# Kernel tuning notes

Hardware: AMD Instinct MI355X
Metric: run time of the kernel (lower is better)

## Reference

```python
import jax, jax.numpy as jnp
import numpy as np

N, D, M, E, K = 16384, 512, 1024, 8, 2
LOSS_COEF = 0.01
EPS = 1e-10


def setup_inputs() -> dict:
    key = jax.random.key(0)
    ks = jax.random.split(key, 6)
    x = jax.random.normal(ks[0], (N, D), dtype=jnp.float32)
    # gate weight (torch init is zeros; use small random so routing is non-degenerate)
    w_gate = 0.02 * jax.random.normal(ks[1], (D, E), dtype=jnp.float32)
    # stacked expert FFN params: Linear(D->M), GELU, Linear(M->D)
    W1 = jax.random.normal(ks[2], (E, D, M), dtype=jnp.float32) / np.sqrt(D)
    b1 = jnp.zeros((E, M), dtype=jnp.float32)
    W2 = jax.random.normal(ks[3], (E, M, D), dtype=jnp.float32) / np.sqrt(M)
    b2 = jnp.zeros((E, D), dtype=jnp.float32)
    return {"x": x, "w_gate": w_gate, "W1": W1, "b1": b1, "W2": W2, "b2": b2}


def _cv_squared(v):
    # torch .var() is unbiased (ddof=1)
    v = v.astype(jnp.float32)
    return jnp.var(v, ddof=1) / (jnp.mean(v) ** 2 + EPS)


def reference(x, w_gate, W1, b1, W2, b2):
    n = x.shape[0]
    # --- noisy_top_k_gating (eval path: no noise) ---
    logits = x @ w_gate                                  # [N, E]
    top_logits, top_idx = jax.lax.top_k(logits, min(K + 1, E))
    topk_logits = top_logits[:, :K]                      # [N, K]
    topk_idx = top_idx[:, :K]                            # [N, K]
    topk_gates = jax.nn.softmax(topk_logits, axis=-1)    # [N, K]
    gates = jnp.zeros_like(logits).at[jnp.arange(n)[:, None], topk_idx].set(topk_gates)
    importance = gates.sum(axis=0)                       # [E]
    load = (gates > 0).sum(axis=0).astype(jnp.float32)   # [E]
    loss = LOSS_COEF * (_cv_squared(importance) + _cv_squared(load))
    # --- experts (dense equivalent of sparse dispatch/combine: gate==0 rows contribute 0) ---
    h = jnp.einsum('nd,edm->enm', x, W1) + b1[:, None, :]     # [E, N, M]
    h = jax.nn.gelu(h, approximate=False)
    out = jnp.einsum('enm,emd->end', h, W2) + b2[:, None, :]  # [E, N, D]
    y = jnp.einsum('ne,end->nd', gates, out)                  # [N, D]
    return (y, loss)
```

## Files before the change

### kernel.cpp

```cpp
#include <hip/hip_runtime.h>
#include <math.h>

#define NTOK 16384
#define DDIM 512
#define MDIM 1024
#define NEXP 8
#define BKW 32
#define TMAX 264

typedef __attribute__((ext_vector_type(8))) short short8;
typedef __attribute__((ext_vector_type(4))) float floatx4;

__device__ inline unsigned short f2bf(float f){
  union { float f; unsigned int u; } v; v.f = f;
  unsigned int u = v.u;
  u += ((u >> 16) & 1u) + 0x7fffu;
  return (unsigned short)(u >> 16);
}

__device__ inline float bf2f(unsigned short s){
  union { unsigned int u; float f; } v;
  v.u = ((unsigned int)s) << 16;
  return v.f;
}

__device__ inline float gelu_fast(float x){
  float u = x * 0.70710678118654752f;
  float a = fabsf(u);
  float t = __builtin_amdgcn_rcpf(fmaf(0.3275911f, a, 1.0f));
  float p = fmaf(1.061405429f, t, -1.453152027f);
  p = fmaf(p, t, 1.421413741f);
  p = fmaf(p, t, -0.284496736f);
  p = fmaf(p, t, 0.254829592f);
  p = p * t;
  float e = __expf(-u * u);
  float erfa = fmaf(-p, e, 1.0f);
  float erfu = copysignf(erfa, u);
  return 0.5f * x * (1.0f + erfu);
}

__device__ __forceinline__ void gload16(const unsigned short* g, unsigned short* l){
  __builtin_amdgcn_global_load_lds(
      (const __attribute__((address_space(1))) void*)g,
      (__attribute__((address_space(3))) void*)l,
      16, 0, 0);
}


__global__ void init_small_kernel(int* counts, float* imp){
  int t = threadIdx.x;
  if (t < NEXP){ counts[t] = 0; imp[t] = 0.0f; }
}

__global__ void transpose_conv_kernel(const float* __restrict__ in,
                                      unsigned short* __restrict__ out,
                                      int R, int C){
  __shared__ float tile[32][33];
  int e  = blockIdx.z;
  int c0 = blockIdx.x << 5;
  int r0 = blockIdx.y << 5;
  const float* src = in + (size_t)e * R * C;
  unsigned short* dst = out + (size_t)e * R * C;
  int tc = threadIdx.x;
  int tr = threadIdx.y;
  #pragma unroll
  for (int i = 0; i < 32; i += 8)
    tile[tr + i][tc] = src[(size_t)(r0 + tr + i) * C + c0 + tc];
  __syncthreads();
  #pragma unroll
  for (int i = 0; i < 32; i += 8)
    dst[(size_t)(c0 + tr + i) * R + r0 + tc] = f2bf(tile[tc][tr + i]);
}


__global__ __launch_bounds__(256)
void gating_kernel(const float* __restrict__ x,
                   const float* __restrict__ wg,
                   unsigned short* __restrict__ xb,
                   int* __restrict__ tok_e, float* __restrict__ tok_g,
                   int* __restrict__ counts, float* __restrict__ imp){
  __shared__ int   lcnt[NEXP];
  __shared__ float limp[NEXP];
  int t = threadIdx.x;
  if (t < NEXP){ lcnt[t] = 0; limp[t] = 0.0f; }
  __syncthreads();

  int wave = t >> 6;
  int lane = t & 63;

  for (int it = 0; it < 4; it++){
    int n = blockIdx.x * 16 + it * 4 + wave;

    const float4* xp = (const float4*)(x + (size_t)n * DDIM + lane * 8);
    float4 a = xp[0], b = xp[1];
    float xv[8] = {a.x, a.y, a.z, a.w, b.x, b.y, b.z, b.w};

    short8 xo;
    #pragma unroll
    for (int j = 0; j < 8; j++) xo[j] = (short)f2bf(xv[j]);
    *(short8*)(xb + (size_t)n * DDIM + lane * 8) = xo;

    double acc[NEXP];
    #pragma unroll
    for (int e = 0; e < NEXP; e++) acc[e] = 0.0;
    #pragma unroll
    for (int j = 0; j < 8; j++){
      const float* wr = wg + (size_t)(lane * 8 + j) * NEXP;
      #pragma unroll
      for (int e = 0; e < NEXP; e++) acc[e] += (double)xv[j] * (double)wr[e];
    }
    #pragma unroll
    for (int off = 32; off >= 1; off >>= 1){
      #pragma unroll
      for (int e = 0; e < NEXP; e++) acc[e] += __shfl_xor(acc[e], off);
    }
    if (lane == 0){
      int i0 = -1, i1 = -1;
      double l0 = -1e300, l1 = -1e300;
      #pragma unroll
      for (int e = 0; e < NEXP; e++){
        double v = acc[e];
        if (v > l0){ l1 = l0; i1 = i0; l0 = v; i0 = e; }
        else if (v > l1){ l1 = v; i1 = e; }
      }
      float ex = expf((float)(l1 - l0));
      float g0 = 1.0f / (1.0f + ex);
      float g1 = ex / (1.0f + ex);
      tok_e[n * 2]     = i0; tok_e[n * 2 + 1] = i1;
      tok_g[n * 2]     = g0; tok_g[n * 2 + 1] = g1;
      atomicAdd(&lcnt[i0], 1); atomicAdd(&lcnt[i1], 1);
      atomicAdd(&limp[i0], g0); atomicAdd(&limp[i1], g1);
    }
  }
  __syncthreads();
  if (t < NEXP){
    atomicAdd(&counts[t], lcnt[t]);
    atomicAdd(&imp[t], limp[t]);
  }
}

__global__ void loss_scan_kernel(const int* __restrict__ counts,
                                 const float* __restrict__ imp,
                                 int* __restrict__ offsets, int* __restrict__ cursor,
                                 int* __restrict__ tile_pre,
                                 float* __restrict__ out_loss){
  int off = 0, tp = 0;
  double si = 0, si2 = 0, sl = 0, sl2 = 0;
  for (int e = 0; e < NEXP; e++){
    offsets[e] = off; cursor[e] = off;
    tile_pre[e] = tp;
    tp += (counts[e] + 127) >> 7;
    off += counts[e];
    double im = (double)imp[e];
    double ld = (double)counts[e];
    si += im; si2 += im * im;
    sl += ld; sl2 += ld * ld;
  }
  offsets[NEXP] = off;
  tile_pre[NEXP] = tp;
  double mi = si / 8.0, ml = sl / 8.0;
  double vi = (si2 - 8.0 * mi * mi) / 7.0;
  double vl = (sl2 - 8.0 * ml * ml) / 7.0;
  double loss = 0.01 * (vi / (mi * mi + 1e-10) + vl / (ml * ml + 1e-10));
  *out_loss = (float)loss;
}

__global__ __launch_bounds__(256)
void scatter_kernel(const int* __restrict__ tok_e,
                    int* __restrict__ cursor,
                    int* __restrict__ btok, int* __restrict__ slot_of){
  __shared__ int lcnt[NEXP];
  __shared__ int lbase[NEXP];
  int t = threadIdx.x;
  if (t < NEXP) lcnt[t] = 0;
  __syncthreads();

  int n = blockIdx.x * 256 + t;
  int e0 = tok_e[n * 2], e1 = tok_e[n * 2 + 1];
  int r0 = atomicAdd(&lcnt[e0], 1);
  int r1 = atomicAdd(&lcnt[e1], 1);
  __syncthreads();
  if (t < NEXP) lbase[t] = atomicAdd(&cursor[t], lcnt[t]);
  __syncthreads();
  int s0 = lbase[e0] + r0;
  int s1 = lbase[e1] + r1;
  btok[s0] = n;
  btok[s1] = n;
  slot_of[n * 2]     = s0;
  slot_of[n * 2 + 1] = s1;
}


__global__ __launch_bounds__(256)
void gemm1_kernel(const unsigned short* __restrict__ xb,
                  const unsigned short* __restrict__ w1t,
                  const float* __restrict__ b1,
                  const int* __restrict__ offsets,
                  const int* __restrict__ tile_pre,
                  const int* __restrict__ btok,
                  unsigned short* __restrict__ H){
  int b = blockIdx.x;
  int L = (b & 7) * TMAX + (b >> 3);
  int ct = L & 7;
  int tt = L >> 3;
  if (tt >= tile_pre[NEXP]) return;
  int e = 0;
  while (tt >= tile_pre[e + 1]) e++;
  int rt = tt - tile_pre[e];
  int off = offsets[e];
  int cnt = offsets[e + 1] - off;
  int r0 = rt << 7;

  __shared__ unsigned short As[3 * 128 * BKW];
  __shared__ unsigned short Bs[3 * 128 * BKW];

  int t = threadIdx.x;
  int w = t >> 6;
  int l = t & 63;
  int lrow = l >> 2;
  int g = (l & 3) ^ ((l >> 3) & 3);

  const unsigned short* apt0;
  const unsigned short* apt1;
  {
    int ra0 = r0 + w * 16 + lrow;        if (ra0 >= cnt) ra0 = cnt - 1;
    int ra1 = r0 + 64 + w * 16 + lrow;   if (ra1 >= cnt) ra1 = cnt - 1;
    apt0 = xb + (size_t)btok[off + ra0] * DDIM + g * 8;
    apt1 = xb + (size_t)btok[off + ra1] * DDIM + g * 8;
  }
  const unsigned short* bpt0 = w1t + ((size_t)e * MDIM + (ct << 7) + w * 16 + lrow) * DDIM + g * 8;
  const unsigned short* bpt1 = bpt0 + (size_t)64 * DDIM;

  int lane = t & 63;
  int wr = (w >> 1) << 6;
  int wc = (w & 1) << 6;
  int lm = lane & 15;
  int lq = lane >> 4;
  int swz = (lm >> 1) & 3;

  int aoff[4], boff[4];
  #pragma unroll
  for (int i = 0; i < 4; i++){
    aoff[i] = (wr + i * 16 + lm) * BKW + ((lq ^ swz) << 3);
    boff[i] = (wc + i * 16 + lm) * BKW + ((lq ^ swz) << 3);
  }

  floatx4 acc[4][4] = {};

  #define STAGE1(K0, CB) {                                   \
    unsigned short* Ac = As + (CB) * 4096;                   \
    unsigned short* Bc = Bs + (CB) * 4096;                   \
    gload16(apt0 + (K0), Ac + w * 512);                      \
    gload16(apt1 + (K0), Ac + 2048 + w * 512);               \
    gload16(bpt0 + (K0), Bc + w * 512);                      \
    gload16(bpt1 + (K0), Bc + 2048 + w * 512);               \
  }
  #define READ1(CB) {                                        \
    const unsigned short* Ac = As + (CB) * 4096;             \
    const unsigned short* Bc = Bs + (CB) * 4096;             \
    _Pragma("unroll")                                        \
    for (int i = 0; i < 4; i++) af[i]  = *(const short8*)(Ac + aoff[i]); \
    _Pragma("unroll")                                        \
    for (int j = 0; j < 4; j++) bfr[j] = *(const short8*)(Bc + boff[j]); \
  }
  #define MFMA1 {                                            \
    _Pragma("unroll")                                        \
    for (int i = 0; i < 4; i++)                              \
      _Pragma("unroll")                                      \
      for (int j = 0; j < 4; j++)                            \
        acc[i][j] = __builtin_amdgcn_mfma_f32_16x16x32_bf16(af[i], bfr[j], acc[i][j], 0, 0, 0); \
  }
  #define WAITBAR(N) {                                       \
    asm volatile("s_waitcnt vmcnt(" #N ")" ::: "memory");    \
    __builtin_amdgcn_sched_barrier(0);                       \
    __builtin_amdgcn_s_barrier();                            \
    __builtin_amdgcn_sched_barrier(0);                       \
  }

  const int NK = DDIM / BKW;
  STAGE1(0, 0);
  STAGE1(BKW, 1);
  WAITBAR(4);
  int cur = 0;
  for (int k = 0; k < NK - 2; k++){
    int st = cur + 2; if (st >= 3) st -= 3;
    short8 af[4], bfr[4];
    READ1(cur);
    STAGE1((k + 2) * BKW, st);
    MFMA1;
    WAITBAR(4);
    cur = (cur + 1 == 3) ? 0 : cur + 1;
  }
  {
    short8 af[4], bfr[4];
    READ1(cur);
    MFMA1;
    WAITBAR(0);
    cur = (cur + 1 == 3) ? 0 : cur + 1;
  }
  {
    short8 af[4], bfr[4];
    READ1(cur);
    MFMA1;
  }
  #undef STAGE1
  #undef READ1
  #undef MFMA1
  #undef WAITBAR

  const float* bias = b1 + e * MDIM + (ct << 7);
  #pragma unroll
  for (int i = 0; i < 4; i++){
    int rbase = wr + i * 16 + lq * 4;
    #pragma unroll
    for (int j = 0; j < 4; j++){
      int cc = wc + j * 16 + lm;
      float bv = bias[cc];
      #pragma unroll
      for (int r = 0; r < 4; r++){
        int row = r0 + rbase + r;
        if (row < cnt){
          float v = acc[i][j][r] + bv;
          H[(size_t)(off + row) * MDIM + (ct << 7) + cc] = f2bf(gelu_fast(v));
        }
      }
    }
  }
}

__global__ __launch_bounds__(256)
void gemm2_kernel(const unsigned short* __restrict__ H,
                  const unsigned short* __restrict__ w2t,
                  const float* __restrict__ b2,
                  const int* __restrict__ offsets,
                  const int* __restrict__ tile_pre,
                  unsigned short* __restrict__ O){
  int b = blockIdx.x;
  int L = (b & 7) * (TMAX / 2) + (b >> 3);
  int ct = L & 3;
  int tt = L >> 2;
  if (tt >= tile_pre[NEXP]) return;
  int e = 0;
  while (tt >= tile_pre[e + 1]) e++;
  int rt = tt - tile_pre[e];
  int off = offsets[e];
  int cnt = offsets[e + 1] - off;
  int r0 = rt << 7;

  __shared__ unsigned short As[3 * 128 * BKW];
  __shared__ unsigned short Bs[3 * 128 * BKW];

  int t = threadIdx.x;
  int w = t >> 6;
  int l = t & 63;
  int lrow = l >> 2;
  int g = (l & 3) ^ ((l >> 3) & 3);

  const unsigned short* apt0;
  const unsigned short* apt1;
  {
    int ra0 = r0 + w * 16 + lrow;        if (ra0 >= cnt) ra0 = cnt - 1;
    int ra1 = r0 + 64 + w * 16 + lrow;   if (ra1 >= cnt) ra1 = cnt - 1;
    apt0 = H + (size_t)(off + ra0) * MDIM + g * 8;
    apt1 = H + (size_t)(off + ra1) * MDIM + g * 8;
  }
  const unsigned short* bpt0 = w2t + ((size_t)e * DDIM + (ct << 7) + w * 16 + lrow) * MDIM + g * 8;
  const unsigned short* bpt1 = bpt0 + (size_t)64 * MDIM;

  int lane = t & 63;
  int wr = (w >> 1) << 6;
  int wc = (w & 1) << 6;
  int lm = lane & 15;
  int lq = lane >> 4;
  int swz = (lm >> 1) & 3;

  int aoff[4], boff[4];
  #pragma unroll
  for (int i = 0; i < 4; i++){
    aoff[i] = (wr + i * 16 + lm) * BKW + ((lq ^ swz) << 3);
    boff[i] = (wc + i * 16 + lm) * BKW + ((lq ^ swz) << 3);
  }

  floatx4 acc[4][4] = {};

  #define STAGE2(K0, CB) {                                   \
    unsigned short* Ac = As + (CB) * 4096;                   \
    unsigned short* Bc = Bs + (CB) * 4096;                   \
    gload16(apt0 + (K0), Ac + w * 512);                      \
    gload16(apt1 + (K0), Ac + 2048 + w * 512);               \
    gload16(bpt0 + (K0), Bc + w * 512);                      \
    gload16(bpt1 + (K0), Bc + 2048 + w * 512);               \
  }
  #define READ2(CB) {                                        \
    const unsigned short* Ac = As + (CB) * 4096;             \
    const unsigned short* Bc = Bs + (CB) * 4096;             \
    _Pragma("unroll")                                        \
    for (int i = 0; i < 4; i++) af[i]  = *(const short8*)(Ac + aoff[i]); \
    _Pragma("unroll")                                        \
    for (int j = 0; j < 4; j++) bfr[j] = *(const short8*)(Bc + boff[j]); \
  }
  #define MFMA2 {                                            \
    _Pragma("unroll")                                        \
    for (int i = 0; i < 4; i++)                              \
      _Pragma("unroll")                                      \
      for (int j = 0; j < 4; j++)                            \
        acc[i][j] = __builtin_amdgcn_mfma_f32_16x16x32_bf16(af[i], bfr[j], acc[i][j], 0, 0, 0); \
  }
  #define WAITBAR2(N) {                                      \
    asm volatile("s_waitcnt vmcnt(" #N ")" ::: "memory");    \
    __builtin_amdgcn_sched_barrier(0);                       \
    __builtin_amdgcn_s_barrier();                            \
    __builtin_amdgcn_sched_barrier(0);                       \
  }

  const int NK = MDIM / BKW;
  STAGE2(0, 0);
  STAGE2(BKW, 1);
  WAITBAR2(4);
  int cur = 0;
  for (int k = 0; k < NK - 2; k++){
    int st = cur + 2; if (st >= 3) st -= 3;
    short8 af[4], bfr[4];
    READ2(cur);
    STAGE2((k + 2) * BKW, st);
    MFMA2;
    WAITBAR2(4);
    cur = (cur + 1 == 3) ? 0 : cur + 1;
  }
  {
    short8 af[4], bfr[4];
    READ2(cur);
    MFMA2;
    WAITBAR2(0);
    cur = (cur + 1 == 3) ? 0 : cur + 1;
  }
  {
    short8 af[4], bfr[4];
    READ2(cur);
    MFMA2;
  }
  #undef STAGE2
  #undef READ2
  #undef MFMA2
  #undef WAITBAR2

  const float* bias = b2 + e * DDIM + (ct << 7);
  #pragma unroll
  for (int i = 0; i < 4; i++){
    int rbase = wr + i * 16 + lq * 4;
    #pragma unroll
    for (int j = 0; j < 4; j++){
      int cc = wc + j * 16 + lm;
      float bv = bias[cc];
      #pragma unroll
      for (int r = 0; r < 4; r++){
        int row = r0 + rbase + r;
        if (row < cnt)
          O[(size_t)(off + row) * DDIM + (ct << 7) + cc] = f2bf(acc[i][j][r] + bv);
      }
    }
  }
}


__global__ __launch_bounds__(256)
void combine_kernel(const unsigned short* __restrict__ O,
                    const float* __restrict__ tok_g,
                    const int* __restrict__ slot_of,
                    float* __restrict__ y){
  int wave = threadIdx.x >> 6;
  int lane = threadIdx.x & 63;
  int n = blockIdx.x * 4 + wave;
  int s0 = slot_of[n * 2], s1 = slot_of[n * 2 + 1];
  float g0 = tok_g[n * 2], g1 = tok_g[n * 2 + 1];
  short8 a = *(const short8*)(O + (size_t)s0 * DDIM + lane * 8);
  short8 b = *(const short8*)(O + (size_t)s1 * DDIM + lane * 8);
  float4 o0, o1;
  float* po0 = (float*)&o0;
  float* po1 = (float*)&o1;
  #pragma unroll
  for (int j = 0; j < 4; j++){
    po0[j] = g0 * bf2f((unsigned short)a[j]) + g1 * bf2f((unsigned short)b[j]);
    po1[j] = g0 * bf2f((unsigned short)a[j + 4]) + g1 * bf2f((unsigned short)b[j + 4]);
  }
  float4* yp = (float4*)(y + (size_t)n * DDIM + lane * 8);
  yp[0] = o0;
  yp[1] = o1;
}


extern "C" void kernel_launch(void* const* d_in, const int* in_sizes, int n_in,
                              void* d_out, int out_size, void* d_ws, size_t ws_size,
                              hipStream_t stream){
  const float* x  = (const float*)d_in[0];
  const float* wg = (const float*)d_in[1];
  const float* W1 = (const float*)d_in[2];
  const float* b1 = (const float*)d_in[3];
  const float* W2 = (const float*)d_in[4];
  const float* b2 = (const float*)d_in[5];
  float* y = (float*)d_out;

  char* ws = (char*)d_ws;
  size_t o = 0;
  auto alloc = [&](size_t bytes)->char*{
    char* p = ws + o;
    o += (bytes + 255) & ~(size_t)255;
    return p;
  };
  unsigned short* xb   = (unsigned short*)alloc((size_t)NTOK * DDIM * 2);
  unsigned short* w1t  = (unsigned short*)alloc((size_t)NEXP * MDIM * DDIM * 2);
  unsigned short* w2t  = (unsigned short*)alloc((size_t)NEXP * DDIM * MDIM * 2);
  unsigned short* H    = (unsigned short*)alloc((size_t)NTOK * 2 * MDIM * 2);
  unsigned short* O    = (unsigned short*)alloc((size_t)NTOK * 2 * DDIM * 2);
  int*   btok    = (int*)  alloc((size_t)NTOK * 2 * 4);
  int*   slot_of = (int*)  alloc((size_t)NTOK * 2 * 4);
  int*   tok_e   = (int*)  alloc((size_t)NTOK * 2 * 4);
  float* tok_g   = (float*)alloc((size_t)NTOK * 2 * 4);
  int*   counts  = (int*)  alloc(64);
  float* imp     = (float*)alloc(64);
  int*   offsets = (int*)  alloc(64);
  int*   cursor  = (int*)  alloc(64);
  int*   tile_pre= (int*)  alloc(64);

  hipLaunchKernelGGL(init_small_kernel, dim3(1), dim3(64), 0, stream, counts, imp);
  hipLaunchKernelGGL(transpose_conv_kernel, dim3(MDIM / 32, DDIM / 32, NEXP), dim3(32, 8), 0, stream,
                     W1, w1t, DDIM, MDIM);
  hipLaunchKernelGGL(transpose_conv_kernel, dim3(DDIM / 32, MDIM / 32, NEXP), dim3(32, 8), 0, stream,
                     W2, w2t, MDIM, DDIM);
  hipLaunchKernelGGL(gating_kernel, dim3(NTOK / 16), dim3(256), 0, stream,
                     x, wg, xb, tok_e, tok_g, counts, imp);
  hipLaunchKernelGGL(loss_scan_kernel, dim3(1), dim3(1), 0, stream,
                     counts, imp, offsets, cursor, tile_pre, y + (size_t)NTOK * DDIM);
  hipLaunchKernelGGL(scatter_kernel, dim3(NTOK / 256), dim3(256), 0, stream,
                     tok_e, cursor, btok, slot_of);
  hipLaunchKernelGGL(gemm1_kernel, dim3(TMAX * 8), dim3(256), 0, stream,
                     xb, w1t, b1, offsets, tile_pre, btok, H);
  hipLaunchKernelGGL(gemm2_kernel, dim3(TMAX * 4), dim3(256), 0, stream,
                     H, w2t, b2, offsets, tile_pre, O);
  hipLaunchKernelGGL(combine_kernel, dim3(NTOK / 4), dim3(256), 0, stream,
                     O, tok_g, slot_of, y);
}
```

Before: 285.0 us.

## Split GEMM tiles across 8 waves and parallelize loss scan with shuffles

Both grouped GEMM kernels now launch 512 threads (8 waves) per 128x128 tile instead of 256, so each wave computes a 32x64 sub-tile with half the accumulators and issues half the global-to-LDS loads per stage. This cuts per-wave register pressure and is meant to raise occupancy and latency hiding (launch bounds 512,6), at the cost of re-reading B fragments from LDS across more waves. The single-thread loss/prefix-scan kernel is rewritten to use one wavefront with lane shuffles so the per-expert offsets are written in parallel.

```diff
diff --git a/kernel.cpp b/kernel.cpp
--- a/kernel.cpp
+++ b/kernel.cpp
@@ -144,25 +144,32 @@
                                  int* __restrict__ offsets, int* __restrict__ cursor,
                                  int* __restrict__ tile_pre,
                                  float* __restrict__ out_loss){
-  int off = 0, tp = 0;
+  int l = threadIdx.x;
+  int   c  = (l < NEXP) ? counts[l] : 0;
+  float im = (l < NEXP) ? imp[l]    : 0.0f;
+  int   tl = (c + 127) >> 7;
+
+  int poff = 0, ptl = 0;
+  int tot = 0, tott = 0;
   double si = 0, si2 = 0, sl = 0, sl2 = 0;
+  #pragma unroll
   for (int e = 0; e < NEXP; e++){
-    offsets[e] = off; cursor[e] = off;
-    tile_pre[e] = tp;
-    tp += (counts[e] + 127) >> 7;
-    off += counts[e];
-    double im = (double)imp[e];
-    double ld = (double)counts[e];
-    si += im; si2 += im * im;
-    sl += ld; sl2 += ld * ld;
-  }
-  offsets[NEXP] = off;
-  tile_pre[NEXP] = tp;
-  double mi = si / 8.0, ml = sl / 8.0;
-  double vi = (si2 - 8.0 * mi * mi) / 7.0;
-  double vl = (sl2 - 8.0 * ml * ml) / 7.0;
-  double loss = 0.01 * (vi / (mi * mi + 1e-10) + vl / (ml * ml + 1e-10));
-  *out_loss = (float)loss;
+    int   ce = __shfl(c, e);
+    int   te = __shfl(tl, e);
+    float ie = __shfl(im, e);
+    if (e < l){ poff += ce; ptl += te; }
+    tot += ce; tott += te;
+    si += (double)ie; si2 += (double)ie * ie;
+    sl += (double)ce; sl2 += (double)ce * ce;
+  }
+  if (l < NEXP){ offsets[l] = poff; cursor[l] = poff; tile_pre[l] = ptl; }
+  if (l == 0){
+    offsets[NEXP] = tot; tile_pre[NEXP] = tott;
+    double mi = si / 8.0, ml = sl / 8.0;
+    double vi = (si2 - 8.0 * mi * mi) / 7.0;
+    double vl = (sl2 - 8.0 * ml * ml) / 7.0;
+    *out_loss = (float)(0.01 * (vi / (mi * mi + 1e-10) + vl / (ml * ml + 1e-10)));
+  }
 }
 
 __global__ __launch_bounds__(256)
@@ -191,7 +198,7 @@
 }
 
 
-__global__ __launch_bounds__(256)
+__global__ __launch_bounds__(512, 6)
 void gemm1_kernel(const unsigned short* __restrict__ xb,
                   const unsigned short* __restrict__ w1t,
                   const float* __restrict__ b1,
@@ -217,55 +224,44 @@
   int t = threadIdx.x;
   int w = t >> 6;
   int l = t & 63;
-  int lrow = l >> 2;
   int g = (l & 3) ^ ((l >> 3) & 3);
 
-  const unsigned short* apt0;
-  const unsigned short* apt1;
+  const unsigned short* apt;
   {
-    int ra0 = r0 + w * 16 + lrow;        if (ra0 >= cnt) ra0 = cnt - 1;
-    int ra1 = r0 + 64 + w * 16 + lrow;   if (ra1 >= cnt) ra1 = cnt - 1;
-    apt0 = xb + (size_t)btok[off + ra0] * DDIM + g * 8;
-    apt1 = xb + (size_t)btok[off + ra1] * DDIM + g * 8;
-  }
-  const unsigned short* bpt0 = w1t + ((size_t)e * MDIM + (ct << 7) + w * 16 + lrow) * DDIM + g * 8;
-  const unsigned short* bpt1 = bpt0 + (size_t)64 * DDIM;
-
-  int lane = t & 63;
-  int wr = (w >> 1) << 6;
+    int ra = r0 + w * 16 + (l >> 2);  if (ra >= cnt) ra = cnt - 1;
+    apt = xb + (size_t)btok[off + ra] * DDIM + g * 8;
+  }
+  const unsigned short* bpt = w1t + ((size_t)e * MDIM + (ct << 7) + w * 16 + (l >> 2)) * DDIM + g * 8;
+
+  int wr = (w >> 1) << 5;
   int wc = (w & 1) << 6;
-  int lm = lane & 15;
-  int lq = lane >> 4;
+  int lm = l & 15;
+  int lq = l >> 4;
   int swz = (lm >> 1) & 3;
 
-  int aoff[4], boff[4];
-  #pragma unroll
-  for (int i = 0; i < 4; i++){
-    aoff[i] = (wr + i * 16 + lm) * BKW + ((lq ^ swz) << 3);
-    boff[i] = (wc + i * 16 + lm) * BKW + ((lq ^ swz) << 3);
-  }
-
-  floatx4 acc[4][4] = {};
+  int aoff[2], boff[4];
+  #pragma unroll
+  for (int i = 0; i < 2; i++) aoff[i] = (wr + i * 16 + lm) * BKW + ((lq ^ swz) << 3);
+  #pragma unroll
+  for (int j = 0; j < 4; j++) boff[j] = (wc + j * 16 + lm) * BKW + ((lq ^ swz) << 3);
+
+  floatx4 acc[2][4] = {};
 
   #define STAGE1(K0, CB) {                                   \
-    unsigned short* Ac = As + (CB) * 4096;                   \
-    unsigned short* Bc = Bs + (CB) * 4096;                   \
-    gload16(apt0 + (K0), Ac + w * 512);                      \
-    gload16(apt1 + (K0), Ac + 2048 + w * 512);               \
-    gload16(bpt0 + (K0), Bc + w * 512);                      \
-    gload16(bpt1 + (K0), Bc + 2048 + w * 512);               \
+    gload16(apt + (K0), As + (CB) * 4096 + w * 512);         \
+    gload16(bpt + (K0), Bs + (CB) * 4096 + w * 512);         \
   }
   #define READ1(CB) {                                        \
     const unsigned short* Ac = As + (CB) * 4096;             \
     const unsigned short* Bc = Bs + (CB) * 4096;             \
     _Pragma("unroll")                                        \
-    for (int i = 0; i < 4; i++) af[i]  = *(const short8*)(Ac + aoff[i]); \
+    for (int i = 0; i < 2; i++) af[i]  = *(const short8*)(Ac + aoff[i]); \
     _Pragma("unroll")                                        \
     for (int j = 0; j < 4; j++) bfr[j] = *(const short8*)(Bc + boff[j]); \
   }
   #define MFMA1 {                                            \
     _Pragma("unroll")                                        \
-    for (int i = 0; i < 4; i++)                              \
+    for (int i = 0; i < 2; i++)                              \
       _Pragma("unroll")                                      \
       for (int j = 0; j < 4; j++)                            \
         acc[i][j] = __builtin_amdgcn_mfma_f32_16x16x32_bf16(af[i], bfr[j], acc[i][j], 0, 0, 0); \
@@ -280,26 +276,26 @@
   const int NK = DDIM / BKW;
   STAGE1(0, 0);
   STAGE1(BKW, 1);
-  WAITBAR(4);
+  WAITBAR(2);
   int cur = 0;
   for (int k = 0; k < NK - 2; k++){
     int st = cur + 2; if (st >= 3) st -= 3;
-    short8 af[4], bfr[4];
+    short8 af[2], bfr[4];
     READ1(cur);
     STAGE1((k + 2) * BKW, st);
     MFMA1;
-    WAITBAR(4);
+    WAITBAR(2);
     cur = (cur + 1 == 3) ? 0 : cur + 1;
   }
   {
-    short8 af[4], bfr[4];
+    short8 af[2], bfr[4];
     READ1(cur);
     MFMA1;
     WAITBAR(0);
     cur = (cur + 1 == 3) ? 0 : cur + 1;
   }
   {
-    short8 af[4], bfr[4];
+    short8 af[2], bfr[4];
     READ1(cur);
     MFMA1;
   }
@@ -310,7 +306,7 @@
 
   const float* bias = b1 + e * MDIM + (ct << 7);
   #pragma unroll
-  for (int i = 0; i < 4; i++){
+  for (int i = 0; i < 2; i++){
     int rbase = wr + i * 16 + lq * 4;
     #pragma unroll
     for (int j = 0; j < 4; j++){
@@ -328,7 +324,7 @@
   }
 }
 
-__global__ __launch_bounds__(256)
+__global__ __launch_bounds__(512, 6)
 void gemm2_kernel(const unsigned short* __restrict__ H,
                   const unsigned short* __restrict__ w2t,
                   const float* __restrict__ b2,
@@ -353,55 +349,44 @@
   int t = threadIdx.x;
   int w = t >> 6;
   int l = t & 63;
-  int lrow = l >> 2;
   int g = (l & 3) ^ ((l >> 3) & 3);
 
-  const unsigned short* apt0;
-  const unsigned short* apt1;
+  const unsigned short* apt;
   {
-    int ra0 = r0 + w * 16 + lrow;        if (ra0 >= cnt) ra0 = cnt - 1;
-    int ra1 = r0 + 64 + w * 16 + lrow;   if (ra1 >= cnt) ra1 = cnt - 1;
-    apt0 = H + (size_t)(off + ra0) * MDIM + g * 8;
-    apt1 = H + (size_t)(off + ra1) * MDIM + g * 8;
-  }
-  const unsigned short* bpt0 = w2t + ((size_t)e * DDIM + (ct << 7) + w * 16 + lrow) * MDIM + g * 8;
-  const unsigned short* bpt1 = bpt0 + (size_t)64 * MDIM;
-
-  int lane = t & 63;
-  int wr = (w >> 1) << 6;
+    int ra = r0 + w * 16 + (l >> 2);  if (ra >= cnt) ra = cnt - 1;
+    apt = H + (size_t)(off + ra) * MDIM + g * 8;
+  }
+  const unsigned short* bpt = w2t + ((size_t)e * DDIM + (ct << 7) + w * 16 + (l >> 2)) * MDIM + g * 8;
+
+  int wr = (w >> 1) << 5;
   int wc = (w & 1) << 6;
-  int lm = lane & 15;
-  int lq = lane >> 4;
+  int lm = l & 15;
+  int lq = l >> 4;
   int swz = (lm >> 1) & 3;
 
-  int aoff[4], boff[4];
-  #pragma unroll
-  for (int i = 0; i < 4; i++){
-    aoff[i] = (wr + i * 16 + lm) * BKW + ((lq ^ swz) << 3);
-    boff[i] = (wc + i * 16 + lm) * BKW + ((lq ^ swz) << 3);
-  }
-
-  floatx4 acc[4][4] = {};
+  int aoff[2], boff[4];
+  #pragma unroll
+  for (int i = 0; i < 2; i++) aoff[i] = (wr + i * 16 + lm) * BKW + ((lq ^ swz) << 3);
+  #pragma unroll
+  for (int j = 0; j < 4; j++) boff[j] = (wc + j * 16 + lm) * BKW + ((lq ^ swz) << 3);
+
+  floatx4 acc[2][4] = {};
 
   #define STAGE2(K0, CB) {                                   \
-    unsigned short* Ac = As + (CB) * 4096;                   \
-    unsigned short* Bc = Bs + (CB) * 4096;                   \
-    gload16(apt0 + (K0), Ac + w * 512);                      \
-    gload16(apt1 + (K0), Ac + 2048 + w * 512);               \
-    gload16(bpt0 + (K0), Bc + w * 512);                      \
-    gload16(bpt1 + (K0), Bc + 2048 + w * 512);               \
+    gload16(apt + (K0), As + (CB) * 4096 + w * 512);         \
+    gload16(bpt + (K0), Bs + (CB) * 4096 + w * 512);         \
   }
   #define READ2(CB) {                                        \
     const unsigned short* Ac = As + (CB) * 4096;             \
     const unsigned short* Bc = Bs + (CB) * 4096;             \
     _Pragma("unroll")                                        \
-    for (int i = 0; i < 4; i++) af[i]  = *(const short8*)(Ac + aoff[i]); \
+    for (int i = 0; i < 2; i++) af[i]  = *(const short8*)(Ac + aoff[i]); \
     _Pragma("unroll")                                        \
     for (int j = 0; j < 4; j++) bfr[j] = *(const short8*)(Bc + boff[j]); \
   }
   #define MFMA2 {                                            \
     _Pragma("unroll")                                        \
-    for (int i = 0; i < 4; i++)                              \
+    for (int i = 0; i < 2; i++)                              \
       _Pragma("unroll")                                      \
       for (int j = 0; j < 4; j++)                            \
         acc[i][j] = __builtin_amdgcn_mfma_f32_16x16x32_bf16(af[i], bfr[j], acc[i][j], 0, 0, 0); \
@@ -416,26 +401,26 @@
   const int NK = MDIM / BKW;
   STAGE2(0, 0);
   STAGE2(BKW, 1);
-  WAITBAR2(4);
+  WAITBAR2(2);
   int cur = 0;
   for (int k = 0; k < NK - 2; k++){
     int st = cur + 2; if (st >= 3) st -= 3;
-    short8 af[4], bfr[4];
+    short8 af[2], bfr[4];
     READ2(cur);
     STAGE2((k + 2) * BKW, st);
     MFMA2;
-    WAITBAR2(4);
+    WAITBAR2(2);
     cur = (cur + 1 == 3) ? 0 : cur + 1;
   }
   {
-    short8 af[4], bfr[4];
+    short8 af[2], bfr[4];
     READ2(cur);
     MFMA2;
     WAITBAR2(0);
     cur = (cur + 1 == 3) ? 0 : cur + 1;
   }
   {
-    short8 af[4], bfr[4];
+    short8 af[2], bfr[4];
     READ2(cur);
     MFMA2;
   }
@@ -446,7 +431,7 @@
 
   const float* bias = b2 + e * DDIM + (ct << 7);
   #pragma unroll
-  for (int i = 0; i < 4; i++){
+  for (int i = 0; i < 2; i++){
     int rbase = wr + i * 16 + lq * 4;
     #pragma unroll
     for (int j = 0; j < 4; j++){
@@ -529,13 +514,13 @@
                      W2, w2t, MDIM, DDIM);
   hipLaunchKernelGGL(gating_kernel, dim3(NTOK / 16), dim3(256), 0, stream,
                      x, wg, xb, tok_e, tok_g, counts, imp);
-  hipLaunchKernelGGL(loss_scan_kernel, dim3(1), dim3(1), 0, stream,
+  hipLaunchKernelGGL(loss_scan_kernel, dim3(1), dim3(64), 0, stream,
                      counts, imp, offsets, cursor, tile_pre, y + (size_t)NTOK * DDIM);
   hipLaunchKernelGGL(scatter_kernel, dim3(NTOK / 256), dim3(256), 0, stream,
                      tok_e, cursor, btok, slot_of);
-  hipLaunchKernelGGL(gemm1_kernel, dim3(TMAX * 8), dim3(256), 0, stream,
+  hipLaunchKernelGGL(gemm1_kernel, dim3(TMAX * 8), dim3(512), 0, stream,
                      xb, w1t, b1, offsets, tile_pre, btok, H);
-  hipLaunchKernelGGL(gemm2_kernel, dim3(TMAX * 4), dim3(256), 0, stream,
+  hipLaunchKernelGGL(gemm2_kernel, dim3(TMAX * 4), dim3(512), 0, stream,
                      H, w2t, b2, offsets, tile_pre, O);
   hipLaunchKernelGGL(combine_kernel, dim3(NTOK / 4), dim3(256), 0, stream,
                      O, tok_g, slot_of, y);
```

After: 274.5 us. 3.7% less time.
